# Performance work log

Measured on AMD Instinct MI355X. Metric: run time of the kernel, lower is better.

The kernel has to match this reference:

```python
import jax, jax.numpy as jnp
import numpy as np


def setup_inputs() -> dict:
    key = jax.random.key(0)
    ks = jax.random.split(key, 7)
    B, S, E, N, H = 2, 2048, 1024, 8, 4096
    scale = 0.02
    return {
        "x": jax.random.normal(ks[0], (B, S, E), dtype=jnp.float32),
        "Wr": jax.random.normal(ks[1], (E, N), dtype=jnp.float32) * scale,
        "br": jnp.zeros((N,), dtype=jnp.float32),
        "W1": jax.random.normal(ks[2], (N, E, H), dtype=jnp.float32) * scale,
        "b1": jnp.zeros((N, H), dtype=jnp.float32),
        "W2": jax.random.normal(ks[3], (N, H, E), dtype=jnp.float32) * scale,
        "b2": jnp.zeros((N, E), dtype=jnp.float32),
        "top_k": 2,
    }


def reference(x, Wr, br, W1, b1, W2, b2, top_k):
    # Router: logits [B,S,N], keep top-k, softmax over the kept entries.
    logits = jnp.einsum("bse,en->bsn", x, Wr) + br
    _, idx = jax.lax.top_k(logits, top_k)                      # [B,S,k]
    mask = jax.nn.one_hot(idx, logits.shape[-1], dtype=jnp.bool_).any(-2)  # [B,S,N]
    masked = jnp.where(mask, logits, -jnp.inf)
    weights = jax.nn.softmax(masked, axis=-1)                   # [B,S,N]

    # Dense all-experts FFN (faithful to original): every expert on every token.
    # hid: [B,S,N,H]
    hid = jax.nn.gelu(jnp.einsum("bse,neh->bsnh", x, W1) + b1, approximate=False)
    expert_out = jnp.einsum("bsnh,nhe->bsne", hid, W2) + b2    # [B,S,N,E]
    # dropout is identity in eval mode

    # Weighted combine over experts.
    return jnp.einsum("bsne,bsn->bse", expert_out, weights)
```

## Files before the change

kernel.cpp:

```cpp
#include <hip/hip_runtime.h>
#include <hip/hip_bf16.h>
#include <cmath>
#include <cstdint>


typedef unsigned short u16;
typedef __attribute__((ext_vector_type(8))) short bf16x8;
typedef __attribute__((ext_vector_type(4))) float f32x4;
typedef __attribute__((ext_vector_type(8))) unsigned short us8;
typedef __attribute__((ext_vector_type(4))) unsigned short us4;

#define TOKENS  4096
#define EDIM    1024
#define NEXP    8
#define HDIM    4096
#define MAXROWS 8192
#define ROWPAD  128
#define MAXTILES 72
#define RBLK    1024

__device__ __forceinline__ u16 f2bf(float f) {
  __hip_bfloat16 h = __float2bfloat16(f);
  return *reinterpret_cast<u16*>(&h);
}
__device__ __forceinline__ int clampk(int k) {
  return k < 1 ? 1 : (k > 8 ? 8 : k);
}
__device__ __forceinline__ void async16(void* lds, const void* g) {
  __builtin_amdgcn_global_load_lds((const __attribute__((address_space(1))) void*)g,
                                   (__attribute__((address_space(3))) void*)lds,
                                   16, 0, 0);
}

__global__ void router_k(const float* __restrict__ x, const float* __restrict__ Wr,
                         const float* __restrict__ br, const int* __restrict__ topk_p,
                         int* __restrict__ sel_e, float* __restrict__ sel_w,
                         int* __restrict__ sel_lpos, int* __restrict__ hist_blk) {
  __shared__ int wsel[4][8];
  const int blk = blockIdx.x;
  const int tid = threadIdx.x;
  const int wv = tid >> 6, ln = tid & 63;
  const int t = blk * 4 + wv;
  const int k = clampk(topk_p[0]);
  float acc[NEXP];
#pragma unroll
  for (int n = 0; n < NEXP; ++n) acc[n] = 0.f;
  const float* xr = x + (size_t)t * EDIM;
  for (int ei = ln; ei < EDIM; ei += 64) {
    float xv = xr[ei];
    float4 w0 = *(const float4*)(Wr + ei * NEXP);
    float4 w1 = *(const float4*)(Wr + ei * NEXP + 4);
    acc[0] += xv * w0.x; acc[1] += xv * w0.y; acc[2] += xv * w0.z; acc[3] += xv * w0.w;
    acc[4] += xv * w1.x; acc[5] += xv * w1.y; acc[6] += xv * w1.z; acc[7] += xv * w1.w;
  }
#pragma unroll
  for (int s = 32; s > 0; s >>= 1) {
#pragma unroll
    for (int n = 0; n < NEXP; ++n) acc[n] += __shfl_down(acc[n], s);
  }
  if (ln == 0) {
    float logit[NEXP];
#pragma unroll
    for (int n = 0; n < NEXP; ++n) logit[n] = acc[n] + br[n];
    bool used[NEXP];
#pragma unroll
    for (int n = 0; n < NEXP; ++n) used[n] = false;
    int se[NEXP]; float sw[NEXP];
    for (int j = 0; j < k; ++j) {
      int bi = 0; float bv = -INFINITY;
      for (int n = 0; n < NEXP; ++n)
        if (!used[n] && logit[n] > bv) { bv = logit[n]; bi = n; }
      used[bi] = true; se[j] = bi; sw[j] = bv;
    }
    float mx = sw[0], sum = 0.f;
    for (int j = 0; j < k; ++j) { sw[j] = expf(sw[j] - mx); sum += sw[j]; }
    float inv = 1.f / sum;
    for (int j = 0; j < k; ++j) {
      sel_e[t * 8 + j] = se[j];
      sel_w[t * 8 + j] = sw[j] * inv;
      wsel[wv][j] = se[j];
    }
  }
  __syncthreads();
  if (tid == 0) {
    int h[NEXP];
#pragma unroll
    for (int e = 0; e < NEXP; ++e) h[e] = 0;
    for (int w = 0; w < 4; ++w)
      for (int j = 0; j < k; ++j) {
        int e = wsel[w][j];
        sel_lpos[(blk * 4 + w) * 8 + j] = h[e]++;
      }
#pragma unroll
    for (int e = 0; e < NEXP; ++e) hist_blk[blk * NEXP + e] = h[e];
  }
}

__global__ void scan_k(const int* __restrict__ hist_blk, int* __restrict__ counts,
                       int* __restrict__ offsets, int* __restrict__ blk_base,
                       int* __restrict__ tmap) {
  __shared__ int sc[NEXP][257];
  __shared__ int offs[NEXP];
  const int tid = threadIdx.x;
  int h[4][NEXP], part[NEXP];
#pragma unroll
  for (int e = 0; e < NEXP; ++e) part[e] = 0;
#pragma unroll
  for (int r = 0; r < 4; ++r) {
    const int row = tid * 4 + r;
#pragma unroll
    for (int e = 0; e < NEXP; ++e) { h[r][e] = hist_blk[row * NEXP + e]; part[e] += h[r][e]; }
  }
#pragma unroll
  for (int e = 0; e < NEXP; ++e) sc[e][tid] = part[e];
  __syncthreads();
  for (int d = 1; d < 256; d <<= 1) {
    int v[NEXP];
#pragma unroll
    for (int e = 0; e < NEXP; ++e) v[e] = (tid >= d) ? sc[e][tid - d] : 0;
    __syncthreads();
#pragma unroll
    for (int e = 0; e < NEXP; ++e) sc[e][tid] += v[e];
    __syncthreads();
  }
  if (tid == 0) {
    int s = 0;
    for (int e = 0; e < NEXP; ++e) {
      int tot = sc[e][255];
      offsets[e] = s; offs[e] = s; counts[e] = tot; s += tot;
    }
    int nt = 0;
    for (int e = 0; e < NEXP; ++e) {
      int nb = (counts[e] + 127) >> 7;
      for (int b = 0; b < nb && nt < MAXTILES; ++b) tmap[nt++] = (e << 16) | b;
    }
    for (; nt < MAXTILES; ++nt) tmap[nt] = -1;
  }
  __syncthreads();
#pragma unroll
  for (int e = 0; e < NEXP; ++e) {
    int run = offs[e] + sc[e][tid] - part[e];
#pragma unroll
    for (int r = 0; r < 4; ++r) {
      blk_base[(tid * 4 + r) * NEXP + e] = run;
      run += h[r][e];
    }
  }
}

__global__ void finalize_k(const int* __restrict__ sel_e, const int* __restrict__ sel_lpos,
                           const int* __restrict__ blk_base, const int* __restrict__ topk_p,
                           int* __restrict__ sel_pos, int* __restrict__ row_token) {
  const int k = clampk(topk_p[0]);
  const int i = blockIdx.x * 256 + threadIdx.x;
  if (i >= TOKENS * k) return;
  const int t = i / k, j = i - t * k;
  const int e = sel_e[t * 8 + j];
  const int pos = blk_base[(t >> 2) * NEXP + e] + sel_lpos[t * 8 + j];
  sel_pos[t * 8 + j] = pos;
  row_token[pos] = t;
}

__global__ void gather_cast_k(const float* __restrict__ x, const int* __restrict__ row_token,
                              const int* __restrict__ counts, u16* __restrict__ xg) {
  __shared__ int tot_s;
  if (threadIdx.x == 0) {
    int t = 0;
#pragma unroll
    for (int e = 0; e < NEXP; ++e) t += counts[e];
    tot_s = t;
  }
  __syncthreads();
  const int row = blockIdx.x;
  if (row >= tot_s) return;
  const float* src = x + (size_t)row_token[row] * EDIM;
  u16* dst = xg + (size_t)row * EDIM;
  const int i = threadIdx.x;
  float4 v = *(const float4*)(src + i * 4);
  us4 o; o[0] = f2bf(v.x); o[1] = f2bf(v.y); o[2] = f2bf(v.z); o[3] = f2bf(v.w);
  *(us4*)(dst + i * 4) = o;
}

__global__ void transpose_k(const float* __restrict__ W1, const float* __restrict__ W2,
                            u16* __restrict__ W1t, u16* __restrict__ W2t,
                            int full, int h0c) {
  __shared__ __align__(16) u16 T[64][68];
  const int z = blockIdx.z;
  int mat, e, h0;
  if (full) { mat = z < 32 ? 0 : 1; int zz = mat ? z - 32 : z; e = zz >> 2; h0 = (zz & 3) * 1024; }
  else      { mat = z < 8 ? 0 : 1;  e = mat ? z - 8 : z;      h0 = h0c; }
  const size_t oes = full ? (size_t)HDIM * EDIM : (size_t)1024 * 1024;
  const float* in; size_t istride;
  if (mat == 0) { in = W1 + (size_t)e * EDIM * HDIM + h0;            istride = HDIM; }
  else          { in = W2 + (size_t)e * HDIM * EDIM + (size_t)h0 * EDIM; istride = EDIM; }
  const int r0 = blockIdx.y * 64, c0 = blockIdx.x * 64;
  const int tid = threadIdx.x;
#pragma unroll
  for (int it = 0; it < 4; ++it) {
    int cell = it * 256 + tid;
    int rl = cell >> 4, c4 = (cell & 15) * 4;
    float4 v = *(const float4*)(in + (size_t)(r0 + rl) * istride + c0 + c4);
    us4 o; o[0] = f2bf(v.x); o[1] = f2bf(v.y); o[2] = f2bf(v.z); o[3] = f2bf(v.w);
    *(us4*)&T[rl][c4] = o;
  }
  __syncthreads();
#pragma unroll
  for (int it = 0; it < 2; ++it) {
    int cell = it * 256 + tid;
    int cl = cell >> 3, r8 = (cell & 7) * 8;
    us8 o;
#pragma unroll
    for (int j = 0; j < 8; ++j) o[j] = T[r8 + j][cl];
    u16* out;
    if (mat == 0) {
      int orow = (full ? h0 : 0) + c0 + cl;
      out = W1t + (size_t)e * oes + (size_t)orow * 1024 + r0 + r8;
    } else {
      int ost = full ? HDIM : 1024;
      out = W2t + (size_t)e * oes + (size_t)(c0 + cl) * ost + (full ? h0 : 0) + r0 + r8;
    }
    *(us8*)out = o;
  }
}

template <int MODE>
__global__ __launch_bounds__(256, 4) void gemm_k(
    const u16* __restrict__ A, int astride,
    const u16* __restrict__ Bt, size_t b_estride, int bstride, int kblocks,
    const float* __restrict__ bias, int bias_dim, int bias_col0,
    const int* __restrict__ counts, const int* __restrict__ offsets,
    const int* __restrict__ tmap,
    u16* __restrict__ hid, int hid_stride, float* __restrict__ Y, int accum, int NB) {
  const int bid = blockIdx.x;
  const int n0i = bid % NB, tile = bid / NB;
  const int tv = tmap[tile];
  if (tv < 0) return;
  const int e = tv >> 16;
  const int m0 = (tv & 0xffff) << 7;
  const int cnt = counts[e], off_e = offsets[e];
  const int n0 = n0i << 7;

  __shared__ __align__(16) u16 As[4096];
  __shared__ __align__(16) u16 Bs[4096];

  const int tid = threadIdx.x;
  const int wv = tid >> 6, ln = tid & 63;

  const int srow = wv * 16 + (ln >> 2);
  const int scol = (ln & 3) * 8;
  const u16* gA0 = A + (size_t)(off_e + m0 + srow) * astride + scol;
  const u16* gA1 = gA0 + (size_t)64 * astride;
  const u16* gB0 = Bt + (size_t)e * b_estride + (size_t)(n0 + srow) * bstride + scol;
  const u16* gB1 = gB0 + (size_t)64 * bstride;
  u16* lA0 = As + wv * 512;  u16* lA1 = As + 2048 + wv * 512;
  u16* lB0 = Bs + wv * 512;  u16* lB1 = Bs + 2048 + wv * 512;

  const int wm = wv >> 1, wn = wv & 1;
  const int quad = ln >> 4, l15 = ln & 15;
  int aoff[4], boff[4];
#pragma unroll
  for (int mi = 0; mi < 4; ++mi) {
    aoff[mi] = (wm * 64 + mi * 16 + l15) * 32 + quad * 8;
    boff[mi] = (wn * 64 + mi * 16 + l15) * 32 + quad * 8;
  }

  f32x4 acc[4][4];
#pragma unroll
  for (int mi = 0; mi < 4; ++mi)
#pragma unroll
    for (int ni = 0; ni < 4; ++ni) acc[mi][ni] = (f32x4){0.f, 0.f, 0.f, 0.f};

  for (int kb = 0; kb < kblocks; ++kb) {
    const int k0 = kb * 32;
    __syncthreads();
    async16(lA0, gA0 + k0);
    async16(lA1, gA1 + k0);
    async16(lB0, gB0 + k0);
    async16(lB1, gB1 + k0);
    __syncthreads();
    bf16x8 a[4], b[4];
#pragma unroll
    for (int mi = 0; mi < 4; ++mi) a[mi] = *(const bf16x8*)(As + aoff[mi]);
#pragma unroll
    for (int ni = 0; ni < 4; ++ni) b[ni] = *(const bf16x8*)(Bs + boff[ni]);
#pragma unroll
    for (int mi = 0; mi < 4; ++mi)
#pragma unroll
      for (int ni = 0; ni < 4; ++ni)
        acc[mi][ni] = __builtin_amdgcn_mfma_f32_16x16x32_bf16(a[mi], b[ni], acc[mi][ni], 0, 0, 0);
  }

#pragma unroll
  for (int mi = 0; mi < 4; ++mi) {
    const int mbase = m0 + wm * 64 + mi * 16 + quad * 4;
#pragma unroll
    for (int ni = 0; ni < 4; ++ni) {
      const int nloc = n0 + wn * 64 + ni * 16 + l15;
      const float bv0 = bias[e * bias_dim + bias_col0 + nloc];
      const float bv = (MODE == 1 && accum) ? 0.f : bv0;
#pragma unroll
      for (int r = 0; r < 4; ++r) {
        const int m = mbase + r;
        if (m < cnt) {
          float v = acc[mi][ni][r] + bv;
          if (MODE == 0) {
            v = 0.5f * v * (1.f + erff(v * 0.70710678118654752f));
            hid[(size_t)(off_e + m) * hid_stride + nloc] = f2bf(v);
          } else {
            size_t yi = (size_t)(off_e + m) * EDIM + nloc;
            Y[yi] = accum ? (Y[yi] + v) : v;
          }
        }
      }
    }
  }
}

__global__ void combine_k(const float* __restrict__ Y, const int* __restrict__ sel_pos,
                          const float* __restrict__ sel_w, const int* __restrict__ topk_p,
                          float* __restrict__ out) {
  const int t = blockIdx.x;
  const int tid = threadIdx.x;
  const int k = clampk(topk_p[0]);
  float a0 = 0.f, a1 = 0.f, a2 = 0.f, a3 = 0.f;
  for (int j = 0; j < k; ++j) {
    const float w = sel_w[t * 8 + j];
    const size_t row = (size_t)sel_pos[t * 8 + j];
    const float4 v = *(const float4*)(Y + row * EDIM + tid * 4);
    a0 += w * v.x; a1 += w * v.y; a2 += w * v.z; a3 += w * v.w;
  }
  float4 o; o.x = a0; o.y = a1; o.z = a2; o.w = a3;
  *(float4*)(out + (size_t)t * EDIM + tid * 4) = o;
}

extern "C" void kernel_launch(void* const* d_in, const int* in_sizes, int n_in,
                              void* d_out, int out_size, void* d_ws, size_t ws_size,
                              hipStream_t stream) {
  const float* x   = (const float*)d_in[0];
  const float* Wr  = (const float*)d_in[1];
  const float* br  = (const float*)d_in[2];
  const float* W1  = (const float*)d_in[3];
  const float* b1  = (const float*)d_in[4];
  const float* W2  = (const float*)d_in[5];
  const float* b2  = (const float*)d_in[6];
  const int* topk  = (const int*)d_in[7];
  float* out = (float*)d_out;

  char* ws = (char*)d_ws;
  size_t o = 0;
  auto alloc = [&](size_t bytes) -> char* {
    char* p = ws + o; o += (bytes + 255) & ~(size_t)255; return p;
  };
  int*   counts    = (int*)alloc(NEXP * 4);
  int*   offsets   = (int*)alloc(NEXP * 4);
  int*   tmap      = (int*)alloc(MAXTILES * 4);
  int*   sel_e     = (int*)alloc((size_t)TOKENS * 8 * 4);
  int*   sel_pos   = (int*)alloc((size_t)TOKENS * 8 * 4);
  int*   sel_lpos  = (int*)alloc((size_t)TOKENS * 8 * 4);
  float* sel_w     = (float*)alloc((size_t)TOKENS * 8 * 4);
  int*   row_token = (int*)alloc((size_t)TOKENS * 8 * 4);
  int*   hist_blk  = (int*)alloc((size_t)RBLK * NEXP * 4);
  int*   blk_base  = (int*)alloc((size_t)RBLK * NEXP * 4);
  u16*   xg        = (u16*)alloc((size_t)(MAXROWS + ROWPAD) * EDIM * 2);
  float* Y         = (float*)alloc((size_t)MAXROWS * EDIM * 4);

  const size_t full_need  = ((size_t)NEXP * HDIM * EDIM * 2) * 2
                          + (size_t)(MAXROWS + ROWPAD) * HDIM * 2 + 4096;
  const size_t chunk_need = ((size_t)NEXP * 1024 * 1024 * 2) * 2
                          + (size_t)(MAXROWS + ROWPAD) * 1024 * 2 + 4096;
  const bool full = (ws_size - o) >= full_need;
  u16 *W1t, *W2t, *hid;
  if (full) {
    W1t = (u16*)alloc((size_t)NEXP * HDIM * EDIM * 2);
    W2t = (u16*)alloc((size_t)NEXP * HDIM * EDIM * 2);
    hid = (u16*)alloc((size_t)(MAXROWS + ROWPAD) * HDIM * 2);
  } else {
    W1t = (u16*)alloc((size_t)NEXP * 1024 * 1024 * 2);
    W2t = (u16*)alloc((size_t)NEXP * 1024 * 1024 * 2);
    hid = (u16*)alloc((size_t)(MAXROWS + ROWPAD) * 1024 * 2);
    (void)chunk_need;
  }

  router_k<<<dim3(RBLK), dim3(256), 0, stream>>>(x, Wr, br, topk,
                                                 sel_e, sel_w, sel_lpos, hist_blk);
  scan_k<<<dim3(1), dim3(256), 0, stream>>>(hist_blk, counts, offsets, blk_base, tmap);
  finalize_k<<<dim3(TOKENS * 8 / 256), dim3(256), 0, stream>>>(sel_e, sel_lpos, blk_base,
                                                               topk, sel_pos, row_token);
  gather_cast_k<<<dim3(MAXROWS), dim3(256), 0, stream>>>(x, row_token, counts, xg);

  if (full) {
    transpose_k<<<dim3(16, 16, 64), dim3(256), 0, stream>>>(W1, W2, W1t, W2t, 1, 0);
    gemm_k<0><<<dim3(MAXTILES * 32), dim3(256), 0, stream>>>(
        xg, EDIM, W1t, (size_t)HDIM * EDIM, 1024, 32,
        b1, HDIM, 0, counts, offsets, tmap, hid, HDIM, nullptr, 0, 32);
    gemm_k<1><<<dim3(MAXTILES * 8), dim3(256), 0, stream>>>(
        hid, HDIM, W2t, (size_t)HDIM * EDIM, HDIM, 128,
        b2, EDIM, 0, counts, offsets, tmap, nullptr, 0, Y, 0, 8);
  } else {
    for (int c = 0; c < 4; ++c) {
      const int h0 = c * 1024;
      transpose_k<<<dim3(16, 16, 16), dim3(256), 0, stream>>>(W1, W2, W1t, W2t, 0, h0);
      gemm_k<0><<<dim3(MAXTILES * 8), dim3(256), 0, stream>>>(
          xg, EDIM, W1t, (size_t)1024 * 1024, 1024, 32,
          b1, HDIM, h0, counts, offsets, tmap, hid, 1024, nullptr, 0, 8);
      gemm_k<1><<<dim3(MAXTILES * 8), dim3(256), 0, stream>>>(
          hid, 1024, W2t, (size_t)1024 * 1024, 1024, 32,
          b2, EDIM, 0, counts, offsets, tmap, nullptr, 0, Y, c > 0 ? 1 : 0, 8);
    }
  }
  combine_k<<<dim3(TOKENS), dim3(256), 0, stream>>>(Y, sel_pos, sel_w, topk, out);
}
```

Baseline: 625.1 us.

## Replace 128x128 expert GEMM with pipelined 256x256 tile kernel and split-K atomics

Replaces the 128x128, 256-thread expert GEMM with a 256x256-tile, 512-thread kernel. The new kernel double-buffers LDS with XOR swizzling, interleaves loads with MFMA phases under explicit waitcnt, barriers and setprio, and remaps workgroups across XCDs. The second GEMM is split four ways along K and accumulates into a pre-zeroed Y with atomicAdd. The exact erf is replaced by a polynomial GELU approximation, and padding rows of the gathered input are zeroed. The aim is higher MFMA utilisation and more operand reuse; the costs are fewer blocks for the uneven expert loads, the atomic traffic, and an extra zeroing kernel.

```diff
diff --git a/kernel.cpp b/kernel.cpp
--- a/kernel.cpp
+++ b/kernel.cpp
@@ -15,9 +15,11 @@
 #define NEXP    8
 #define HDIM    4096
 #define MAXROWS 8192
-#define ROWPAD  128
-#define MAXTILES 72
+#define ROWPAD  384
+#define MAXTILES 40
 #define RBLK    1024
+
+#define MFMA16(va, vb, vc) __builtin_amdgcn_mfma_f32_16x16x32_bf16(va, vb, vc, 0, 0, 0)
 
 __device__ __forceinline__ u16 f2bf(float f) {
   __hip_bfloat16 h = __float2bfloat16(f);
@@ -30,6 +32,20 @@
   __builtin_amdgcn_global_load_lds((const __attribute__((address_space(1))) void*)g,
                                    (__attribute__((address_space(3))) void*)lds,
                                    16, 0, 0);
+}
+__device__ __forceinline__ float gelu_f(float v) {
+  const float z = fabsf(v) * 0.70710678118654752f;
+  const float t = __builtin_amdgcn_rcpf(fmaf(0.3275911f, z, 1.0f));
+  const float p = t * fmaf(t, fmaf(t, fmaf(t, fmaf(t, 1.061405429f, -1.453152027f),
+                                           1.421413741f), -0.284496736f), 0.254829592f);
+  float er = 1.0f - p * __expf(-z * z);
+  er = copysignf(er, v);
+  return 0.5f * v * (1.0f + er);
+}
+__device__ __forceinline__ int xcd_swz(int orig, int nwg) {
+  const int q = nwg >> 3, r = nwg & 7;
+  const int x = orig & 7, l = orig >> 3;
+  return (x < r ? x * (q + 1) : r * (q + 1) + (x - r) * q) + l;
 }
 
 __global__ void router_k(const float* __restrict__ x, const float* __restrict__ Wr,
@@ -131,7 +147,7 @@
     }
     int nt = 0;
     for (int e = 0; e < NEXP; ++e) {
-      int nb = (counts[e] + 127) >> 7;
+      int nb = (counts[e] + 255) >> 8;
       for (int b = 0; b < nb && nt < MAXTILES; ++b) tmap[nt++] = (e << 16) | b;
     }
     for (; nt < MAXTILES; ++nt) tmap[nt] = -1;
@@ -172,13 +188,23 @@
   }
   __syncthreads();
   const int row = blockIdx.x;
-  if (row >= tot_s) return;
-  const float* src = x + (size_t)row_token[row] * EDIM;
   u16* dst = xg + (size_t)row * EDIM;
   const int i = threadIdx.x;
+  if (row >= tot_s) {
+    us4 z = {0, 0, 0, 0};
+    *(us4*)(dst + i * 4) = z;
+    return;
+  }
+  const float* src = x + (size_t)row_token[row] * EDIM;
   float4 v = *(const float4*)(src + i * 4);
   us4 o; o[0] = f2bf(v.x); o[1] = f2bf(v.y); o[2] = f2bf(v.z); o[3] = f2bf(v.w);
   *(us4*)(dst + i * 4) = o;
+}
+
+__global__ void zero_f32_k(float* __restrict__ p) {
+  const size_t i = ((size_t)blockIdx.x * 256 + threadIdx.x) * 4;
+  float4 z = {0.f, 0.f, 0.f, 0.f};
+  *(float4*)(p + i) = z;
 }
 
 __global__ void transpose_k(const float* __restrict__ W1, const float* __restrict__ W2,
@@ -224,91 +250,185 @@
 }
 
 template <int MODE>
-__global__ __launch_bounds__(256, 4) void gemm_k(
-    const u16* __restrict__ A, int astride,
-    const u16* __restrict__ Bt, size_t b_estride, int bstride, int kblocks,
-    const float* __restrict__ bias, int bias_dim, int bias_col0,
+__global__ __launch_bounds__(512, 2) void gemm256_k(
+    const u16* __restrict__ A, int astride, int kblocks,
+    const u16* __restrict__ Bt, size_t b_estride, int bstride,
+    const float* __restrict__ bias, int bias_dim, int bias_col0, int bias_on,
     const int* __restrict__ counts, const int* __restrict__ offsets,
-    const int* __restrict__ tmap,
-    u16* __restrict__ hid, int hid_stride, float* __restrict__ Y, int accum, int NB) {
-  const int bid = blockIdx.x;
-  const int n0i = bid % NB, tile = bid / NB;
+    const int* __restrict__ tmap, int NB,
+    u16* __restrict__ hid, int hid_stride, float* __restrict__ Y) {
+  __shared__ __align__(16) char lds_s[131072];
+  const int bid = xcd_swz(blockIdx.x, gridDim.x);
+  const int by  = blockIdx.y;
+  const int tile = bid / NB;
   const int tv = tmap[tile];
   if (tv < 0) return;
+  const int n0 = (bid - tile * NB) << 8;
   const int e = tv >> 16;
-  const int m0 = (tv & 0xffff) << 7;
+  const int m0 = (tv & 0xffff) << 8;
   const int cnt = counts[e], off_e = offsets[e];
-  const int n0 = n0i << 7;
-
-  __shared__ __align__(16) u16 As[4096];
-  __shared__ __align__(16) u16 Bs[4096];
 
   const int tid = threadIdx.x;
   const int wv = tid >> 6, ln = tid & 63;
-
-  const int srow = wv * 16 + (ln >> 2);
-  const int scol = (ln & 3) * 8;
-  const u16* gA0 = A + (size_t)(off_e + m0 + srow) * astride + scol;
-  const u16* gA1 = gA0 + (size_t)64 * astride;
-  const u16* gB0 = Bt + (size_t)e * b_estride + (size_t)(n0 + srow) * bstride + scol;
-  const u16* gB1 = gB0 + (size_t)64 * bstride;
-  u16* lA0 = As + wv * 512;  u16* lA1 = As + 2048 + wv * 512;
-  u16* lB0 = Bs + wv * 512;  u16* lB1 = Bs + 2048 + wv * 512;
-
-  const int wm = wv >> 1, wn = wv & 1;
-  const int quad = ln >> 4, l15 = ln & 15;
-  int aoff[4], boff[4];
-#pragma unroll
-  for (int mi = 0; mi < 4; ++mi) {
-    aoff[mi] = (wm * 64 + mi * 16 + l15) * 32 + quad * 8;
-    boff[mi] = (wn * 64 + mi * 16 + l15) * 32 + quad * 8;
-  }
-
-  f32x4 acc[4][4];
-#pragma unroll
-  for (int mi = 0; mi < 4; ++mi)
-#pragma unroll
-    for (int ni = 0; ni < 4; ++ni) acc[mi][ni] = (f32x4){0.f, 0.f, 0.f, 0.f};
-
-  for (int kb = 0; kb < kblocks; ++kb) {
-    const int k0 = kb * 32;
-    __syncthreads();
-    async16(lA0, gA0 + k0);
-    async16(lA1, gA1 + k0);
-    async16(lB0, gB0 + k0);
-    async16(lB1, gB1 + k0);
-    __syncthreads();
-    bf16x8 a[4], b[4];
-#pragma unroll
-    for (int mi = 0; mi < 4; ++mi) a[mi] = *(const bf16x8*)(As + aoff[mi]);
-#pragma unroll
-    for (int ni = 0; ni < 4; ++ni) b[ni] = *(const bf16x8*)(Bs + boff[ni]);
+  const int wm = wv >> 2, wn = wv & 3;
+
+  const int trow = tid >> 3;
+  const int swz  = (tid & 7) ^ (trow & 7);
+  const size_t koff = (size_t)by * kblocks * 64;
+  const u16* gA = A + (size_t)(off_e + m0 + trow) * astride + koff + swz * 8;
+  const u16* gB = Bt + (size_t)e * b_estride + (size_t)(n0 + trow) * bstride + koff + swz * 8;
+  const size_t a64 = (size_t)astride * 64;
+  const size_t b64 = (size_t)bstride * 64;
+  char* const lA = lds_s + wv * 1024;
+  char* const lB = lds_s + 65536 + wv * 1024;
+
+  auto stA = [&](int buf, int h, int kt) {
+    const u16* g = gA + (size_t)(2 * h) * a64 + (size_t)kt * 64;
+    char* l = lA + (buf << 15) + (h << 14);
+    async16(l, g);
+    async16(l + 8192, g + a64);
+  };
+  auto stB = [&](int buf, int h, int kt) {
+    const u16* g = gB + (size_t)(2 * h) * b64 + (size_t)kt * 64;
+    char* l = lB + (buf << 15) + (h << 14);
+    async16(l, g);
+    async16(l + 8192, g + b64);
+  };
+
+  const int r15 = ln & 15, quad = ln >> 4, rs = r15 & 7;
+  const int a_k0 = (wm * 128 + r15) * 128 + (((quad    ) ^ rs) << 4);
+  const int a_k1 = (wm * 128 + r15) * 128 + (((quad + 4) ^ rs) << 4);
+  const int b_k0 = (wn *  64 + r15) * 128 + (((quad    ) ^ rs) << 4);
+  const int b_k1 = (wn *  64 + r15) * 128 + (((quad + 4) ^ rs) << 4);
+
+  f32x4 acc[8][4];
+#pragma unroll
+  for (int i = 0; i < 8; ++i)
+#pragma unroll
+    for (int j = 0; j < 4; ++j) acc[i][j] = (f32x4){0.f, 0.f, 0.f, 0.f};
+
+  bf16x8 a0[4], a1[4], b0[4], b1[4];
+
+  stB(0, 0, 0); stB(0, 1, 0);
+  stA(0, 0, 0); stA(0, 1, 0);
+  if (kblocks > 1) {
+    stB(1, 0, 1); stB(1, 1, 1);
+    asm volatile("s_waitcnt vmcnt(4)" ::: "memory");
+  } else {
+    asm volatile("s_waitcnt vmcnt(0)" ::: "memory");
+  }
+  __builtin_amdgcn_s_barrier();
+
+  for (int t = 0; t < kblocks; ++t) {
+    const int cb = (t & 1) << 15;
+    const int nx = (t & 1) ^ 1;
+    const char* cA = lds_s + cb;
+    const char* cB = lds_s + 65536 + cb;
+
+#pragma unroll
+    for (int mi = 0; mi < 4; ++mi) {
+      a0[mi] = *(const bf16x8*)(cA + a_k0 + mi * 2048);
+      a1[mi] = *(const bf16x8*)(cA + a_k1 + mi * 2048);
+    }
+#pragma unroll
+    for (int ni = 0; ni < 2; ++ni) {
+      b0[ni] = *(const bf16x8*)(cB + b_k0 + ni * 2048);
+      b1[ni] = *(const bf16x8*)(cB + b_k1 + ni * 2048);
+    }
+    if (t + 1 < kblocks) stA(nx, 0, t + 1);
+    asm volatile("s_waitcnt lgkmcnt(8)" ::: "memory");
+    __builtin_amdgcn_s_barrier();
+    asm volatile("s_waitcnt lgkmcnt(0)" ::: "memory");
+    __builtin_amdgcn_s_setprio(1);
 #pragma unroll
     for (int mi = 0; mi < 4; ++mi)
 #pragma unroll
-      for (int ni = 0; ni < 4; ++ni)
-        acc[mi][ni] = __builtin_amdgcn_mfma_f32_16x16x32_bf16(a[mi], b[ni], acc[mi][ni], 0, 0, 0);
-  }
-
-#pragma unroll
-  for (int mi = 0; mi < 4; ++mi) {
-    const int mbase = m0 + wm * 64 + mi * 16 + quad * 4;
+      for (int ni = 0; ni < 2; ++ni) {
+        acc[mi][ni] = MFMA16(a0[mi], b0[ni], acc[mi][ni]);
+        acc[mi][ni] = MFMA16(a1[mi], b1[ni], acc[mi][ni]);
+      }
+    __builtin_amdgcn_s_setprio(0);
+    __builtin_amdgcn_s_barrier();
+
+#pragma unroll
+    for (int ni = 2; ni < 4; ++ni) {
+      b0[ni] = *(const bf16x8*)(cB + b_k0 + ni * 2048);
+      b1[ni] = *(const bf16x8*)(cB + b_k1 + ni * 2048);
+    }
+    if (t + 1 < kblocks) stA(nx, 1, t + 1);
+    __builtin_amdgcn_s_barrier();
+    asm volatile("s_waitcnt lgkmcnt(0)" ::: "memory");
+    __builtin_amdgcn_s_setprio(1);
+#pragma unroll
+    for (int mi = 0; mi < 4; ++mi)
+#pragma unroll
+      for (int ni = 2; ni < 4; ++ni) {
+        acc[mi][ni] = MFMA16(a0[mi], b0[ni], acc[mi][ni]);
+        acc[mi][ni] = MFMA16(a1[mi], b1[ni], acc[mi][ni]);
+      }
+    __builtin_amdgcn_s_setprio(0);
+    __builtin_amdgcn_s_barrier();
+
+#pragma unroll
+    for (int mi = 0; mi < 4; ++mi) {
+      a0[mi] = *(const bf16x8*)(cA + a_k0 + (mi + 4) * 2048);
+      a1[mi] = *(const bf16x8*)(cA + a_k1 + (mi + 4) * 2048);
+    }
+    if (t + 2 < kblocks) stB(t & 1, 0, t + 2);
+    __builtin_amdgcn_s_barrier();
+    asm volatile("s_waitcnt lgkmcnt(0)" ::: "memory");
+    __builtin_amdgcn_s_setprio(1);
+#pragma unroll
+    for (int mi = 0; mi < 4; ++mi)
+#pragma unroll
+      for (int ni = 0; ni < 2; ++ni) {
+        acc[mi + 4][ni] = MFMA16(a0[mi], b0[ni], acc[mi + 4][ni]);
+        acc[mi + 4][ni] = MFMA16(a1[mi], b1[ni], acc[mi + 4][ni]);
+      }
+    __builtin_amdgcn_s_setprio(0);
+    __builtin_amdgcn_s_barrier();
+
+    if (t + 2 < kblocks) {
+      stB(t & 1, 1, t + 2);
+      asm volatile("s_waitcnt vmcnt(4)" ::: "memory");
+    } else {
+      asm volatile("s_waitcnt vmcnt(0)" ::: "memory");
+    }
+    __builtin_amdgcn_s_barrier();
+    __builtin_amdgcn_s_setprio(1);
+#pragma unroll
+    for (int mi = 0; mi < 4; ++mi)
+#pragma unroll
+      for (int ni = 2; ni < 4; ++ni) {
+        acc[mi + 4][ni] = MFMA16(a0[mi], b0[ni], acc[mi + 4][ni]);
+        acc[mi + 4][ni] = MFMA16(a1[mi], b1[ni], acc[mi + 4][ni]);
+      }
+    __builtin_amdgcn_s_setprio(0);
+    __builtin_amdgcn_s_barrier();
+  }
+
+  const int col0 = n0 + wn * 64 + r15;
+  float bv[4];
+#pragma unroll
+  for (int ni = 0; ni < 4; ++ni) {
+    const float b = bias[(size_t)e * bias_dim + bias_col0 + col0 + ni * 16];
+    bv[ni] = (MODE == 0) ? b : ((bias_on && by == 0) ? b : 0.f);
+  }
+#pragma unroll
+  for (int mi = 0; mi < 8; ++mi) {
+    const int mb = m0 + wm * 128 + mi * 16 + quad * 4;
 #pragma unroll
     for (int ni = 0; ni < 4; ++ni) {
-      const int nloc = n0 + wn * 64 + ni * 16 + l15;
-      const float bv0 = bias[e * bias_dim + bias_col0 + nloc];
-      const float bv = (MODE == 1 && accum) ? 0.f : bv0;
+      const int nc = col0 + ni * 16;
 #pragma unroll
       for (int r = 0; r < 4; ++r) {
-        const int m = mbase + r;
+        const int m = mb + r;
         if (m < cnt) {
-          float v = acc[mi][ni][r] + bv;
+          const float v = acc[mi][ni][r] + bv[ni];
           if (MODE == 0) {
-            v = 0.5f * v * (1.f + erff(v * 0.70710678118654752f));
-            hid[(size_t)(off_e + m) * hid_stride + nloc] = f2bf(v);
+            hid[(size_t)(off_e + m) * hid_stride + nc] = f2bf(gelu_f(v));
           } else {
-            size_t yi = (size_t)(off_e + m) * EDIM + nloc;
-            Y[yi] = accum ? (Y[yi] + v) : v;
+            atomicAdd(&Y[(size_t)(off_e + m) * EDIM + nc], v);
           }
         }
       }
@@ -366,8 +486,6 @@
 
   const size_t full_need  = ((size_t)NEXP * HDIM * EDIM * 2) * 2
                           + (size_t)(MAXROWS + ROWPAD) * HDIM * 2 + 4096;
-  const size_t chunk_need = ((size_t)NEXP * 1024 * 1024 * 2) * 2
-                          + (size_t)(MAXROWS + ROWPAD) * 1024 * 2 + 4096;
   const bool full = (ws_size - o) >= full_need;
   u16 *W1t, *W2t, *hid;
   if (full) {
@@ -378,34 +496,34 @@
     W1t = (u16*)alloc((size_t)NEXP * 1024 * 1024 * 2);
     W2t = (u16*)alloc((size_t)NEXP * 1024 * 1024 * 2);
     hid = (u16*)alloc((size_t)(MAXROWS + ROWPAD) * 1024 * 2);
-    (void)chunk_need;
-  }
-
+  }
+
+  zero_f32_k<<<dim3((MAXROWS * EDIM) / 1024), dim3(256), 0, stream>>>(Y);
   router_k<<<dim3(RBLK), dim3(256), 0, stream>>>(x, Wr, br, topk,
                                                  sel_e, sel_w, sel_lpos, hist_blk);
   scan_k<<<dim3(1), dim3(256), 0, stream>>>(hist_blk, counts, offsets, blk_base, tmap);
   finalize_k<<<dim3(TOKENS * 8 / 256), dim3(256), 0, stream>>>(sel_e, sel_lpos, blk_base,
                                                                topk, sel_pos, row_token);
-  gather_cast_k<<<dim3(MAXROWS), dim3(256), 0, stream>>>(x, row_token, counts, xg);
+  gather_cast_k<<<dim3(MAXROWS + ROWPAD), dim3(256), 0, stream>>>(x, row_token, counts, xg);
 
   if (full) {
     transpose_k<<<dim3(16, 16, 64), dim3(256), 0, stream>>>(W1, W2, W1t, W2t, 1, 0);
-    gemm_k<0><<<dim3(MAXTILES * 32), dim3(256), 0, stream>>>(
-        xg, EDIM, W1t, (size_t)HDIM * EDIM, 1024, 32,
-        b1, HDIM, 0, counts, offsets, tmap, hid, HDIM, nullptr, 0, 32);
-    gemm_k<1><<<dim3(MAXTILES * 8), dim3(256), 0, stream>>>(
-        hid, HDIM, W2t, (size_t)HDIM * EDIM, HDIM, 128,
-        b2, EDIM, 0, counts, offsets, tmap, nullptr, 0, Y, 0, 8);
+    gemm256_k<0><<<dim3(MAXTILES * 16, 1), dim3(512), 0, stream>>>(
+        xg, EDIM, 16, W1t, (size_t)HDIM * EDIM, EDIM,
+        b1, HDIM, 0, 1, counts, offsets, tmap, 16, hid, HDIM, nullptr);
+    gemm256_k<1><<<dim3(MAXTILES * 4, 4), dim3(512), 0, stream>>>(
+        hid, HDIM, 16, W2t, (size_t)HDIM * EDIM, HDIM,
+        b2, EDIM, 0, 1, counts, offsets, tmap, 4, nullptr, 0, Y);
   } else {
     for (int c = 0; c < 4; ++c) {
       const int h0 = c * 1024;
       transpose_k<<<dim3(16, 16, 16), dim3(256), 0, stream>>>(W1, W2, W1t, W2t, 0, h0);
-      gemm_k<0><<<dim3(MAXTILES * 8), dim3(256), 0, stream>>>(
-          xg, EDIM, W1t, (size_t)1024 * 1024, 1024, 32,
-          b1, HDIM, h0, counts, offsets, tmap, hid, 1024, nullptr, 0, 8);
-      gemm_k<1><<<dim3(MAXTILES * 8), dim3(256), 0, stream>>>(
-          hid, 1024, W2t, (size_t)1024 * 1024, 1024, 32,
-          b2, EDIM, 0, counts, offsets, tmap, nullptr, 0, Y, c > 0 ? 1 : 0, 8);
+      gemm256_k<0><<<dim3(MAXTILES * 4, 1), dim3(512), 0, stream>>>(
+          xg, EDIM, 16, W1t, (size_t)1024 * 1024, 1024,
+          b1, HDIM, h0, 1, counts, offsets, tmap, 4, hid, 1024, nullptr);
+      gemm256_k<1><<<dim3(MAXTILES * 4, 1), dim3(512), 0, stream>>>(
+          hid, 1024, 16, W2t, (size_t)1024 * 1024, 1024,
+          b2, EDIM, 0, (c == 0) ? 1 : 0, counts, offsets, tmap, 4, nullptr, 0, Y);
     }
   }
   combine_k<<<dim3(TOKENS), dim3(256), 0, stream>>>(Y, sel_pos, sel_w, topk, out);
```

Measured after the change: 687.6 us. 10.0% more time.
